# Kernel tuning notes

Hardware: AMD Instinct MI355X
Metric: run time of the kernel (lower is better)

## Reference

```python
import jax, jax.numpy as jnp
import numpy as np
from jax.ops import segment_sum, segment_max

B, L, D, H, DK, NL, V, FF = 8, 256, 256, 8, 32, 4, 2048, 1024
N = B * L
EPS = 1e-5


def _ln(x, g, b):
    m = jnp.mean(x, -1, keepdims=True)
    v = jnp.var(x, -1, keepdims=True)
    return (x - m) * jax.lax.rsqrt(v + EPS) * g + b


def setup_inputs() -> dict:
    key = jax.random.key(0)
    ks = list(jax.random.split(key, 16))
    # causal decoder-decoder edges, sorted by destination (DGL 'dd' eids)
    dst_seq = np.repeat(np.arange(L), np.arange(L) + 1)
    src_seq = np.concatenate([np.arange(j + 1) for j in range(L)])
    src = jnp.asarray(np.concatenate([src_seq + b * L for b in range(B)]), jnp.int32)
    dst = jnp.asarray(np.concatenate([dst_seq + b * L for b in range(B)]), jnp.int32)
    tokens = jax.random.randint(ks[0], (N,), 0, V)
    positions = jnp.tile(jnp.arange(L), B)  # tgt[1]
    s = 0.02
    nrm = lambda k, sh: jax.random.normal(k, sh, jnp.float32) * s
    return {
        'tokens': tokens, 'positions': positions, 'src': src, 'dst': dst,
        'value_tab': nrm(ks[1], (V, D)),
        'coord_tab': nrm(ks[2], (3, D)),
        'pos_tab': nrm(ks[3], (L, D)),
        'ln1_g': jnp.ones((NL, D), jnp.float32), 'ln1_b': jnp.zeros((NL, D), jnp.float32),
        'Wq': nrm(ks[4], (NL, D, D)), 'Wk': nrm(ks[5], (NL, D, D)),
        'Wv': nrm(ks[6], (NL, D, D)), 'Wo': nrm(ks[7], (NL, D, D)),
        'ln2_g': jnp.ones((NL, D), jnp.float32), 'ln2_b': jnp.zeros((NL, D), jnp.float32),
        'W1': nrm(ks[8], (NL, D, FF)), 'b1': jnp.zeros((NL, FF), jnp.float32),
        'W2': nrm(ks[9], (NL, FF, D)), 'b2': jnp.zeros((NL, D), jnp.float32),
        'lnf_g': jnp.ones((D,), jnp.float32), 'lnf_b': jnp.zeros((D,), jnp.float32),
        'Wgen': nrm(ks[10], (D, V)), 'bgen': jnp.zeros((V,), jnp.float32),
    }


def reference(tokens, positions, src, dst, value_tab, coord_tab, pos_tab,
              ln1_g, ln1_b, Wq, Wk, Wv, Wo, ln2_g, ln2_b,
              W1, b1, W2, b2, lnf_g, lnf_b, Wgen, bgen):
    # embeddings: value*sqrt(d) + coord(pos%3) + pos(pos//3)
    x = value_tab[tokens] * jnp.sqrt(jnp.float32(D)) \
        + coord_tab[positions % 3] + pos_tab[positions // 3]
    inv_sqrt_dk = 1.0 / jnp.sqrt(jnp.float32(DK))
    for i in range(NL):
        # pre_func: layernorm + qkv projection, split heads
        xn = _ln(x, ln1_g[i], ln1_b[i])
        q = (xn @ Wq[i]).reshape(N, H, DK)
        k = (xn @ Wk[i]).reshape(N, H, DK)
        v = (xn @ Wv[i]).reshape(N, H, DK)
        # apply_edges(u_dot_v): per-edge, per-head score
        score = jnp.einsum('ehd,ehd->eh', k[src], q[dst]) * inv_sqrt_dk  # [E,H]
        # edge_softmax over edges grouped by destination node
        m = jax.lax.stop_gradient(
            segment_max(score, dst, num_segments=N, indices_are_sorted=True))
        a = jnp.exp(score - m[dst])
        denom = segment_sum(a, dst, num_segments=N, indices_are_sorted=True)
        alpha = a / denom[dst]  # [E,H]
        # send_and_recv(u_mul_e -> sum): softmax-weighted aggregation
        z = segment_sum(v[src] * alpha[..., None], dst,
                        num_segments=N, indices_are_sorted=True).reshape(N, D)
        # post_func: output proj + residual, then FFN sublayer
        x = x + z @ Wo[i]
        xn2 = _ln(x, ln2_g[i], ln2_b[i])
        x = x + (jax.nn.relu(xn2 @ W1[i] + b1[i]) @ W2[i] + b2[i])
    x = _ln(x, lnf_g, lnf_b)
    return jax.nn.log_softmax(x @ Wgen + bgen, axis=-1)  # generator
```

## Files before the change

kernel.cpp:

```cpp
#include <hip/hip_runtime.h>
#include <hip/hip_bf16.h>
#include <math.h>

constexpr int B_ = 8, L_ = 256, D_ = 256, H_ = 8, DK_ = 32, NL_ = 4, V_ = 2048, FF_ = 1024;
constexpr int N_ = B_ * L_;
constexpr float EPS_ = 1e-5f;

typedef short bf16x8 __attribute__((ext_vector_type(8)));
typedef float f32x4 __attribute__((ext_vector_type(4)));
typedef _Float16 f16x4 __attribute__((ext_vector_type(4)));

__device__ __forceinline__ short f2b(float f) {
    union { __hip_bfloat16 h; short s; } u;
    u.h = __float2bfloat16(f);
    return u.s;
}

__device__ __forceinline__ void load16_lds(const void* g, void* l) {
    auto gp = reinterpret_cast<const __attribute__((address_space(1))) unsigned int*>(
        reinterpret_cast<unsigned long long>(g));
    auto lp = reinterpret_cast<__attribute__((address_space(3))) unsigned int*>(
        (unsigned int)reinterpret_cast<unsigned long long>(l));
    __builtin_amdgcn_global_load_lds(gp, lp, 16, 0, 0);
}

__global__ void embed_kernel(const int* __restrict__ tokens, const int* __restrict__ positions,
                             const float* __restrict__ vtab, const float* __restrict__ ctab,
                             const float* __restrict__ ptab, float* __restrict__ x) {
    int n = blockIdx.x, d = threadIdx.x;
    int tok = tokens[n], p = positions[n];
    x[n * D_ + d] = vtab[tok * D_ + d] * 16.0f + ctab[(p % 3) * D_ + d] + ptab[(p / 3) * D_ + d];
}

__global__ void ln_kernel(const float* __restrict__ x, const float* __restrict__ g,
                          const float* __restrict__ b, short* __restrict__ out) {
    __shared__ float r1[4], r2[4], mv[2];
    int n = blockIdx.x, t = threadIdx.x;
    float v = x[n * D_ + t];
    float s1 = v, s2 = v * v;
#pragma unroll
    for (int off = 32; off; off >>= 1) {
        s1 += __shfl_down(s1, off, 64);
        s2 += __shfl_down(s2, off, 64);
    }
    int w = t >> 6;
    if ((t & 63) == 0) { r1[w] = s1; r2[w] = s2; }
    __syncthreads();
    if (t == 0) {
        float a = r1[0] + r1[1] + r1[2] + r1[3];
        float c = r2[0] + r2[1] + r2[2] + r2[3];
        float mean = a * (1.0f / D_);
        float var = c * (1.0f / D_) - mean * mean;
        mv[0] = mean;
        mv[1] = rsqrtf(var + EPS_);
    }
    __syncthreads();
    out[n * D_ + t] = f2b((v - mv[0]) * mv[1] * g[t] + b[t]);
}

__global__ void transpose_w(const float* __restrict__ src, short* __restrict__ dst, int K, int Nn) {
    __shared__ float tile[32][33];
    int n0 = blockIdx.x * 32, k0 = blockIdx.y * 32;
    size_t base = (size_t)blockIdx.z * K * Nn;
    src += base;
    dst += base;
    int tx = threadIdx.x, ty = threadIdx.y;
#pragma unroll
    for (int i = 0; i < 32; i += 8)
        tile[ty + i][tx] = src[(size_t)(k0 + ty + i) * Nn + n0 + tx];
    __syncthreads();
#pragma unroll
    for (int i = 0; i < 32; i += 8)
        dst[(size_t)(n0 + ty + i) * K + k0 + tx] = f2b(tile[tx][ty + i]);
}

__global__ void transpose_w4(const float* __restrict__ Wq, const float* __restrict__ Wk,
                             const float* __restrict__ Wv, const float* __restrict__ Wo,
                             short* __restrict__ wqT, short* __restrict__ wkT,
                             short* __restrict__ wvT, short* __restrict__ woT) {
    __shared__ float tile[32][33];
    int z = blockIdx.z, m = z & 3, layer = z >> 2;
    const float* src = (m == 0) ? Wq : (m == 1) ? Wk : (m == 2) ? Wv : Wo;
    short* dst = (m == 0) ? wqT : (m == 1) ? wkT : (m == 2) ? wvT : woT;
    src += (size_t)layer * D_ * D_;
    dst += (size_t)layer * D_ * D_;
    int n0 = blockIdx.x * 32, k0 = blockIdx.y * 32;
    int tx = threadIdx.x, ty = threadIdx.y;
#pragma unroll
    for (int i = 0; i < 32; i += 8)
        tile[ty + i][tx] = src[(size_t)(k0 + ty + i) * D_ + n0 + tx];
    __syncthreads();
#pragma unroll
    for (int i = 0; i < 32; i += 8)
        dst[(size_t)(n0 + ty + i) * D_ + k0 + tx] = f2b(tile[tx][ty + i]);
}

template <int EPI, bool HAS_BIAS>
__device__ __forceinline__ void gemm_body(short (*As)[64], short (*Bs)[64],
                                          const short* __restrict__ A, const short* __restrict__ Bt,
                                          const float* __restrict__ bias, float* __restrict__ Cf,
                                          short* __restrict__ Cb, int M, int K, int Nout,
                                          int kbeg, int kend, int kz) {
    int t = threadIdx.x;
    int m0 = blockIdx.x * 64, n0 = blockIdx.y * 64;
    int lane = t & 63, w = t >> 6;
    int mo = (w & 1) * 32, no = (w >> 1) * 32;
    int quad = lane >> 4, r = lane & 15;
    f32x4 acc00 = {}, acc01 = {}, acc10 = {}, acc11 = {};
    int srow = 16 * w + (lane >> 3);
    int scol = (lane & 7) * 8;
    const short* Ag = &A[(size_t)(m0 + srow) * K + scol];
    const short* Bg = &Bt[(size_t)(n0 + srow) * K + scol];
    for (int k0 = kbeg; k0 < kend; k0 += 64) {
        __syncthreads();
        load16_lds(Ag + k0, &As[16 * w][0]);
        load16_lds(Ag + (size_t)8 * K + k0, &As[16 * w + 8][0]);
        load16_lds(Bg + k0, &Bs[16 * w][0]);
        load16_lds(Bg + (size_t)8 * K + k0, &Bs[16 * w + 8][0]);
        __syncthreads();
#pragma unroll
        for (int kk = 0; kk < 64; kk += 32) {
            bf16x8 a0 = *(const bf16x8*)&As[mo + r][kk + quad * 8];
            bf16x8 a1 = *(const bf16x8*)&As[mo + 16 + r][kk + quad * 8];
            bf16x8 b0 = *(const bf16x8*)&Bs[no + r][kk + quad * 8];
            bf16x8 b1 = *(const bf16x8*)&Bs[no + 16 + r][kk + quad * 8];
            acc00 = __builtin_amdgcn_mfma_f32_16x16x32_bf16(a0, b0, acc00, 0, 0, 0);
            acc01 = __builtin_amdgcn_mfma_f32_16x16x32_bf16(a0, b1, acc01, 0, 0, 0);
            acc10 = __builtin_amdgcn_mfma_f32_16x16x32_bf16(a1, b0, acc10, 0, 0, 0);
            acc11 = __builtin_amdgcn_mfma_f32_16x16x32_bf16(a1, b1, acc11, 0, 0, 0);
        }
    }
#pragma unroll
    for (int i = 0; i < 2; ++i) {
#pragma unroll
        for (int j = 0; j < 2; ++j) {
            f32x4 acc = (i == 0) ? (j == 0 ? acc00 : acc01) : (j == 0 ? acc10 : acc11);
            int col = n0 + no + j * 16 + r;
            float bval = HAS_BIAS ? bias[col] : 0.f;
#pragma unroll
            for (int p = 0; p < 4; ++p) {
                int row = m0 + mo + i * 16 + quad * 4 + p;
                float v = acc[p];
                if (EPI == 0) {
                    Cf[(size_t)row * Nout + col] = v;
                } else if (EPI == 1) {
                    Cb[(size_t)row * Nout + col] = f2b(fmaxf(v + bval, 0.f));
                } else if (EPI == 2) {
                    float add = v + ((HAS_BIAS && kz == 0) ? bval : 0.f);
                    atomicAdd(&Cf[(size_t)row * Nout + col], add);
                } else if (EPI == 3) {
                    Cf[(size_t)row * Nout + col] = v + bval;
                } else if (EPI == 4) {
                    Cb[(size_t)row * Nout + col] = f2b(v);
                } else {
                    ((_Float16*)Cb)[(size_t)row * Nout + col] = (_Float16)v;
                }
            }
        }
    }
}

__global__ __launch_bounds__(256) void gemm_qkv(const short* __restrict__ A, const short* __restrict__ wq,
                                                const short* __restrict__ wk, const short* __restrict__ wv,
                                                short* __restrict__ q, short* __restrict__ k,
                                                short* __restrict__ v, int M, int K, int Nout) {
    __shared__ short As[64][64];
    __shared__ short Bs[64][64];
    if (blockIdx.z == 0)
        gemm_body<4, false>(As, Bs, A, wq, nullptr, nullptr, q, M, K, Nout, 0, K, 0);
    else if (blockIdx.z == 1)
        gemm_body<4, false>(As, Bs, A, wk, nullptr, nullptr, k, M, K, Nout, 0, K, 0);
    else
        gemm_body<5, false>(As, Bs, A, wv, nullptr, nullptr, v, M, K, Nout, 0, K, 0);
}

template <int SPLITK, bool HAS_BIAS>
__global__ __launch_bounds__(256) void gemm_accum(const short* __restrict__ A, const short* __restrict__ Bt,
                                                  const float* __restrict__ bias, float* __restrict__ C,
                                                  int M, int K, int Nout) {
    __shared__ short As[64][64];
    __shared__ short Bs[64][64];
    int Kp = K / SPLITK;
    int kz = blockIdx.z;
    gemm_body<2, HAS_BIAS>(As, Bs, A, Bt, bias, C, nullptr, M, K, Nout, kz * Kp, kz * Kp + Kp, kz);
}

__global__ __launch_bounds__(256) void gemm_biasrelu_bf16(const short* __restrict__ A,
                                                          const short* __restrict__ Bt,
                                                          const float* __restrict__ bias,
                                                          short* __restrict__ C, int M, int K, int Nout) {
    __shared__ short As[64][64];
    __shared__ short Bs[64][64];
    gemm_body<1, true>(As, Bs, A, Bt, bias, nullptr, C, M, K, Nout, 0, K, 0);
}

__global__ __launch_bounds__(256) void gemm_bias(const short* __restrict__ A, const short* __restrict__ Bt,
                                                 const float* __restrict__ bias, float* __restrict__ C,
                                                 int M, int K, int Nout) {
    __shared__ short As[64][64];
    __shared__ short Bs[64][64];
    gemm_body<3, true>(As, Bs, A, Bt, bias, C, nullptr, M, K, Nout, 0, K, 0);
}

__global__ __launch_bounds__(64) void attn_kernel(const short* __restrict__ q,
                                                  const short* __restrict__ k,
                                                  const _Float16* __restrict__ v,
                                                  short* __restrict__ z) {
    int blk = blockIdx.x;
    int bh = blk & 63;
    int qt = 15 - (blk >> 6);
    int b = bh >> 3, h = bh & 7;
    int lane = threadIdx.x;
    int r = lane & 15, quad = lane >> 4;
    int row0 = b * L_;

    bf16x8 qf = *(const bf16x8*)&q[(size_t)(row0 + qt * 16 + r) * D_ + h * DK_ + quad * 8];
    f32x4 O0 = {}, O1 = {};
    float mA = -1e30f, den = 0.f;
    int nk = qt + 1;

    bf16x8 kf = *(const bf16x8*)&k[(size_t)(row0 + r) * D_ + h * DK_ + quad * 8];
    f16x4 va, vb;
    {
        const _Float16* vp = v + (size_t)(row0 + quad * 4) * D_ + h * DK_;
#pragma unroll
        for (int i = 0; i < 4; ++i) {
            va[i] = vp[(size_t)i * D_ + r];
            vb[i] = vp[(size_t)i * D_ + 16 + r];
        }
    }
    for (int kt = 0; kt < nk; ++kt) {
        bf16x8 kf_n = kf;
        f16x4 va_n = va, vb_n = vb;
        if (kt + 1 < nk) {
            kf_n = *(const bf16x8*)&k[(size_t)(row0 + (kt + 1) * 16 + r) * D_ + h * DK_ + quad * 8];
            const _Float16* vp = v + (size_t)(row0 + (kt + 1) * 16 + quad * 4) * D_ + h * DK_;
#pragma unroll
            for (int i = 0; i < 4; ++i) {
                va_n[i] = vp[(size_t)i * D_ + r];
                vb_n[i] = vp[(size_t)i * D_ + 16 + r];
            }
        }
        f32x4 zero = {};
        f32x4 s = __builtin_amdgcn_mfma_f32_16x16x32_bf16(kf, qf, zero, 0, 0, 0);
#pragma unroll
        for (int i2 = 0; i2 < 4; ++i2) s[i2] *= 0.17677669529663687f;
        if (kt == qt) {
#pragma unroll
            for (int i2 = 0; i2 < 4; ++i2)
                if (quad * 4 + i2 > r) s[i2] = -1e30f;
        }
        float tmax = fmaxf(fmaxf(s[0], s[1]), fmaxf(s[2], s[3]));
        tmax = fmaxf(tmax, __shfl_xor(tmax, 16, 64));
        tmax = fmaxf(tmax, __shfl_xor(tmax, 32, 64));
        float mn = fmaxf(mA, tmax);
        float alpha = __expf(mA - mn);
        mA = mn;
        float p0 = __expf(s[0] - mn), p1 = __expf(s[1] - mn);
        float p2 = __expf(s[2] - mn), p3 = __expf(s[3] - mn);
        float ts = (p0 + p1) + (p2 + p3);
        ts += __shfl_xor(ts, 16, 64);
        ts += __shfl_xor(ts, 32, 64);
        den = den * alpha + ts;
        f16x4 pf;
        pf[0] = (_Float16)p0; pf[1] = (_Float16)p1; pf[2] = (_Float16)p2; pf[3] = (_Float16)p3;
        float al[4];
#pragma unroll
        for (int i2 = 0; i2 < 4; ++i2) al[i2] = __shfl(alpha, quad * 4 + i2, 64);
#pragma unroll
        for (int i2 = 0; i2 < 4; ++i2) { O0[i2] *= al[i2]; O1[i2] *= al[i2]; }
        O0 = __builtin_amdgcn_mfma_f32_16x16x16f16(pf, va, O0, 0, 0, 0);
        O1 = __builtin_amdgcn_mfma_f32_16x16x16f16(pf, vb, O1, 0, 0, 0);
        kf = kf_n; va = va_n; vb = vb_n;
    }
#pragma unroll
    for (int i2 = 0; i2 < 4; ++i2) {
        float inv = 1.0f / __shfl(den, quad * 4 + i2, 64);
        int rowz = row0 + qt * 16 + quad * 4 + i2;
        z[(size_t)rowz * D_ + h * DK_ + r] = f2b(O0[i2] * inv);
        z[(size_t)rowz * D_ + h * DK_ + 16 + r] = f2b(O1[i2] * inv);
    }
}

__global__ void lsm_kernel(float* __restrict__ logits) {
    __shared__ float rm[4], rs[4];
    int row = blockIdx.x, t = threadIdx.x;
    float* p = logits + (size_t)row * V_;
    float vals[8];
    float mx = -INFINITY;
#pragma unroll
    for (int i = 0; i < 8; ++i) {
        vals[i] = p[t + i * 256];
        mx = fmaxf(mx, vals[i]);
    }
#pragma unroll
    for (int off = 32; off; off >>= 1) mx = fmaxf(mx, __shfl_xor(mx, off, 64));
    int w = t >> 6;
    if ((t & 63) == 0) rm[w] = mx;
    __syncthreads();
    mx = fmaxf(fmaxf(rm[0], rm[1]), fmaxf(rm[2], rm[3]));
    float s = 0.f;
#pragma unroll
    for (int i = 0; i < 8; ++i) s += __expf(vals[i] - mx);
#pragma unroll
    for (int off = 32; off; off >>= 1) s += __shfl_xor(s, off, 64);
    if ((t & 63) == 0) rs[w] = s;
    __syncthreads();
    s = rs[0] + rs[1] + rs[2] + rs[3];
    float lse = mx + logf(s);
#pragma unroll
    for (int i = 0; i < 8; ++i) p[t + i * 256] = vals[i] - lse;
}

extern "C" void kernel_launch(void* const* d_in, const int* in_sizes, int n_in,
                              void* d_out, int out_size, void* d_ws, size_t ws_size,
                              hipStream_t stream) {
    const int* tokens = (const int*)d_in[0];
    const int* positions = (const int*)d_in[1];
    const float* vtab = (const float*)d_in[4];
    const float* ctab = (const float*)d_in[5];
    const float* ptab = (const float*)d_in[6];
    const float* ln1_g = (const float*)d_in[7];
    const float* ln1_b = (const float*)d_in[8];
    const float* Wq = (const float*)d_in[9];
    const float* Wk = (const float*)d_in[10];
    const float* Wv = (const float*)d_in[11];
    const float* Wo = (const float*)d_in[12];
    const float* ln2_g = (const float*)d_in[13];
    const float* ln2_b = (const float*)d_in[14];
    const float* W1 = (const float*)d_in[15];
    const float* b1 = (const float*)d_in[16];
    const float* W2 = (const float*)d_in[17];
    const float* b2 = (const float*)d_in[18];
    const float* lnf_g = (const float*)d_in[19];
    const float* lnf_b = (const float*)d_in[20];
    const float* Wgen = (const float*)d_in[21];
    const float* bgen = (const float*)d_in[22];

    char* p = (char*)d_ws;
    float* x = (float*)p;      p += (size_t)N_ * D_ * 4;
    short* qb = (short*)p;     p += (size_t)N_ * D_ * 4;
    short* kb = (short*)p;     p += (size_t)N_ * D_ * 4;
    short* vbh = (short*)p;    p += (size_t)N_ * D_ * 4;
    short* xnb = (short*)p;    p += (size_t)N_ * D_ * 2;
    short* zbb = (short*)p;    p += (size_t)N_ * D_ * 2;
    short* hbb = (short*)p;    p += (size_t)N_ * FF_ * 2;
    short* wqT = (short*)p;    p += (size_t)NL_ * D_ * D_ * 2;
    short* wkT = (short*)p;    p += (size_t)NL_ * D_ * D_ * 2;
    short* wvT = (short*)p;    p += (size_t)NL_ * D_ * D_ * 2;
    short* woT = (short*)p;    p += (size_t)NL_ * D_ * D_ * 2;
    short* w1T = (short*)p;    p += (size_t)NL_ * D_ * FF_ * 2;
    short* w2T = (short*)p;    p += (size_t)NL_ * FF_ * D_ * 2;
    short* wgT = (short*)p;    p += (size_t)D_ * V_ * 2;
    float* out = (float*)d_out;

    dim3 tb(32, 8);
    transpose_w4<<<dim3(8, 8, 16), tb, 0, stream>>>(Wq, Wk, Wv, Wo, wqT, wkT, wvT, woT);
    transpose_w<<<dim3(32, 8, NL_), tb, 0, stream>>>(W1, w1T, D_, FF_);
    transpose_w<<<dim3(8, 32, NL_), tb, 0, stream>>>(W2, w2T, FF_, D_);
    transpose_w<<<dim3(64, 8, 1), tb, 0, stream>>>(Wgen, wgT, D_, V_);

    embed_kernel<<<N_, 256, 0, stream>>>(tokens, positions, vtab, ctab, ptab, x);
    dim3 gQKV(N_ / 64, D_ / 64, 3);
    dim3 gWo(N_ / 64, D_ / 64, 4);
    dim3 gW1(N_ / 64, FF_ / 64);
    dim3 gW2(N_ / 64, D_ / 64, 8);
    dim3 gGen(N_ / 64, V_ / 64);
    for (int i = 0; i < NL_; ++i) {
        ln_kernel<<<N_, 256, 0, stream>>>(x, ln1_g + i * D_, ln1_b + i * D_, xnb);
        gemm_qkv<<<gQKV, 256, 0, stream>>>(xnb, wqT + (size_t)i * D_ * D_, wkT + (size_t)i * D_ * D_,
                                           wvT + (size_t)i * D_ * D_, qb, kb, vbh, N_, D_, D_);
        attn_kernel<<<B_ * H_ * 16, 64, 0, stream>>>(qb, kb, (const _Float16*)vbh, zbb);
        gemm_accum<4, false><<<gWo, 256, 0, stream>>>(zbb, woT + (size_t)i * D_ * D_, nullptr, x, N_, D_, D_);
        ln_kernel<<<N_, 256, 0, stream>>>(x, ln2_g + i * D_, ln2_b + i * D_, xnb);
        gemm_biasrelu_bf16<<<gW1, 256, 0, stream>>>(xnb, w1T + (size_t)i * D_ * FF_, b1 + (size_t)i * FF_,
                                                    hbb, N_, D_, FF_);
        gemm_accum<8, true><<<gW2, 256, 0, stream>>>(hbb, w2T + (size_t)i * FF_ * D_, b2 + (size_t)i * D_,
                                                     x, N_, FF_, D_);
    }
    ln_kernel<<<N_, 256, 0, stream>>>(x, lnf_g, lnf_b, xnb);
    gemm_bias<<<gGen, 256, 0, stream>>>(xnb, wgT, bgen, out, N_, D_, V_);
    lsm_kernel<<<N_, 256, 0, stream>>>(out);
}
```

Measured before the change: 361.1 us.

## Add 128x128 GEMM for W1/generator, register-prefetch small GEMMs, halve split-K

```diff
diff --git a/kernel.cpp b/kernel.cpp
--- a/kernel.cpp
+++ b/kernel.cpp
@@ -96,10 +96,10 @@
 }
 
 template <int EPI, bool HAS_BIAS>
-__device__ __forceinline__ void gemm_body(short (*As)[64], short (*Bs)[64],
+__device__ __forceinline__ void gemm_body(short (*As)[40], short (*Bs)[40],
                                           const short* __restrict__ A, const short* __restrict__ Bt,
                                           const float* __restrict__ bias, float* __restrict__ Cf,
-                                          short* __restrict__ Cb, int M, int K, int Nout,
+                                          short* __restrict__ Cb, int K, int Nout,
                                           int kbeg, int kend, int kz) {
     int t = threadIdx.x;
     int m0 = blockIdx.x * 64, n0 = blockIdx.y * 64;
@@ -107,28 +107,28 @@
     int mo = (w & 1) * 32, no = (w >> 1) * 32;
     int quad = lane >> 4, r = lane & 15;
     f32x4 acc00 = {}, acc01 = {}, acc10 = {}, acc11 = {};
-    int srow = 16 * w + (lane >> 3);
-    int scol = (lane & 7) * 8;
-    const short* Ag = &A[(size_t)(m0 + srow) * K + scol];
-    const short* Bg = &Bt[(size_t)(n0 + srow) * K + scol];
-    for (int k0 = kbeg; k0 < kend; k0 += 64) {
+    int sr = t >> 2, sc = (t & 3) * 8;
+    const short* Ap = &A[(size_t)(m0 + sr) * K + sc];
+    const short* Bg = &Bt[(size_t)(n0 + sr) * K + sc];
+    int4 aR = *(const int4*)(Ap + kbeg);
+    int4 bR = *(const int4*)(Bg + kbeg);
+    for (int k0 = kbeg; k0 < kend; k0 += 32) {
         __syncthreads();
-        load16_lds(Ag + k0, &As[16 * w][0]);
-        load16_lds(Ag + (size_t)8 * K + k0, &As[16 * w + 8][0]);
-        load16_lds(Bg + k0, &Bs[16 * w][0]);
-        load16_lds(Bg + (size_t)8 * K + k0, &Bs[16 * w + 8][0]);
+        *(int4*)&As[sr][sc] = aR;
+        *(int4*)&Bs[sr][sc] = bR;
         __syncthreads();
-#pragma unroll
-        for (int kk = 0; kk < 64; kk += 32) {
-            bf16x8 a0 = *(const bf16x8*)&As[mo + r][kk + quad * 8];
-            bf16x8 a1 = *(const bf16x8*)&As[mo + 16 + r][kk + quad * 8];
-            bf16x8 b0 = *(const bf16x8*)&Bs[no + r][kk + quad * 8];
-            bf16x8 b1 = *(const bf16x8*)&Bs[no + 16 + r][kk + quad * 8];
-            acc00 = __builtin_amdgcn_mfma_f32_16x16x32_bf16(a0, b0, acc00, 0, 0, 0);
-            acc01 = __builtin_amdgcn_mfma_f32_16x16x32_bf16(a0, b1, acc01, 0, 0, 0);
-            acc10 = __builtin_amdgcn_mfma_f32_16x16x32_bf16(a1, b0, acc10, 0, 0, 0);
-            acc11 = __builtin_amdgcn_mfma_f32_16x16x32_bf16(a1, b1, acc11, 0, 0, 0);
-        }
+        if (k0 + 32 < kend) {
+            aR = *(const int4*)(Ap + k0 + 32);
+            bR = *(const int4*)(Bg + k0 + 32);
+        }
+        bf16x8 a0 = *(const bf16x8*)&As[mo + r][quad * 8];
+        bf16x8 a1 = *(const bf16x8*)&As[mo + 16 + r][quad * 8];
+        bf16x8 b0 = *(const bf16x8*)&Bs[no + r][quad * 8];
+        bf16x8 b1 = *(const bf16x8*)&Bs[no + 16 + r][quad * 8];
+        acc00 = __builtin_amdgcn_mfma_f32_16x16x32_bf16(a0, b0, acc00, 0, 0, 0);
+        acc01 = __builtin_amdgcn_mfma_f32_16x16x32_bf16(a0, b1, acc01, 0, 0, 0);
+        acc10 = __builtin_amdgcn_mfma_f32_16x16x32_bf16(a1, b0, acc10, 0, 0, 0);
+        acc11 = __builtin_amdgcn_mfma_f32_16x16x32_bf16(a1, b1, acc11, 0, 0, 0);
     }
 #pragma unroll
     for (int i = 0; i < 2; ++i) {
@@ -141,15 +141,9 @@
             for (int p = 0; p < 4; ++p) {
                 int row = m0 + mo + i * 16 + quad * 4 + p;
                 float v = acc[p];
-                if (EPI == 0) {
-                    Cf[(size_t)row * Nout + col] = v;
-                } else if (EPI == 1) {
-                    Cb[(size_t)row * Nout + col] = f2b(fmaxf(v + bval, 0.f));
-                } else if (EPI == 2) {
+                if (EPI == 2) {
                     float add = v + ((HAS_BIAS && kz == 0) ? bval : 0.f);
                     atomicAdd(&Cf[(size_t)row * Nout + col], add);
-                } else if (EPI == 3) {
-                    Cf[(size_t)row * Nout + col] = v + bval;
                 } else if (EPI == 4) {
                     Cb[(size_t)row * Nout + col] = f2b(v);
                 } else {
@@ -163,43 +157,83 @@
 __global__ __launch_bounds__(256) void gemm_qkv(const short* __restrict__ A, const short* __restrict__ wq,
                                                 const short* __restrict__ wk, const short* __restrict__ wv,
                                                 short* __restrict__ q, short* __restrict__ k,
-                                                short* __restrict__ v, int M, int K, int Nout) {
-    __shared__ short As[64][64];
-    __shared__ short Bs[64][64];
+                                                short* __restrict__ v, int K, int Nout) {
+    __shared__ short As[64][40];
+    __shared__ short Bs[64][40];
     if (blockIdx.z == 0)
-        gemm_body<4, false>(As, Bs, A, wq, nullptr, nullptr, q, M, K, Nout, 0, K, 0);
+        gemm_body<4, false>(As, Bs, A, wq, nullptr, nullptr, q, K, Nout, 0, K, 0);
     else if (blockIdx.z == 1)
-        gemm_body<4, false>(As, Bs, A, wk, nullptr, nullptr, k, M, K, Nout, 0, K, 0);
+        gemm_body<4, false>(As, Bs, A, wk, nullptr, nullptr, k, K, Nout, 0, K, 0);
     else
-        gemm_body<5, false>(As, Bs, A, wv, nullptr, nullptr, v, M, K, Nout, 0, K, 0);
+        gemm_body<5, false>(As, Bs, A, wv, nullptr, nullptr, v, K, Nout, 0, K, 0);
 }
 
 template <int SPLITK, bool HAS_BIAS>
 __global__ __launch_bounds__(256) void gemm_accum(const short* __restrict__ A, const short* __restrict__ Bt,
                                                   const float* __restrict__ bias, float* __restrict__ C,
-                                                  int M, int K, int Nout) {
-    __shared__ short As[64][64];
-    __shared__ short Bs[64][64];
+                                                  int K, int Nout) {
+    __shared__ short As[64][40];
+    __shared__ short Bs[64][40];
     int Kp = K / SPLITK;
     int kz = blockIdx.z;
-    gemm_body<2, HAS_BIAS>(As, Bs, A, Bt, bias, C, nullptr, M, K, Nout, kz * Kp, kz * Kp + Kp, kz);
-}
-
-__global__ __launch_bounds__(256) void gemm_biasrelu_bf16(const short* __restrict__ A,
-                                                          const short* __restrict__ Bt,
-                                                          const float* __restrict__ bias,
-                                                          short* __restrict__ C, int M, int K, int Nout) {
-    __shared__ short As[64][64];
-    __shared__ short Bs[64][64];
-    gemm_body<1, true>(As, Bs, A, Bt, bias, nullptr, C, M, K, Nout, 0, K, 0);
-}
-
-__global__ __launch_bounds__(256) void gemm_bias(const short* __restrict__ A, const short* __restrict__ Bt,
-                                                 const float* __restrict__ bias, float* __restrict__ C,
-                                                 int M, int K, int Nout) {
-    __shared__ short As[64][64];
-    __shared__ short Bs[64][64];
-    gemm_body<3, true>(As, Bs, A, Bt, bias, C, nullptr, M, K, Nout, 0, K, 0);
+    gemm_body<2, HAS_BIAS>(As, Bs, A, Bt, bias, C, nullptr, K, Nout, kz * Kp, kz * Kp + Kp, kz);
+}
+
+template <int EPI>
+__global__ __launch_bounds__(256) void gemm128(const short* __restrict__ A, const short* __restrict__ Bt,
+                                               const float* __restrict__ bias, float* __restrict__ Cf,
+                                               short* __restrict__ Cb, int K, int Nout) {
+    __shared__ short As[128][64];
+    __shared__ short Bs[128][64];
+    int t = threadIdx.x;
+    int m0 = blockIdx.x * 128, n0 = blockIdx.y * 128;
+    int lane = t & 63, w = t >> 6;
+    int wr = (w & 1) * 64, wc = (w >> 1) * 64;
+    int quad = lane >> 4, r = lane & 15;
+    f32x4 acc[4][4] = {};
+    int srow = lane >> 3, scol = (lane & 7) * 8;
+    const short* Ag = &A[(size_t)(m0 + 32 * w + srow) * K + scol];
+    const short* Bg = &Bt[(size_t)(n0 + 32 * w + srow) * K + scol];
+    for (int k0 = 0; k0 < K; k0 += 64) {
+        __syncthreads();
+#pragma unroll
+        for (int op = 0; op < 4; ++op) {
+            load16_lds(Ag + (size_t)(8 * op) * K + k0, &As[32 * w + 8 * op][0]);
+            load16_lds(Bg + (size_t)(8 * op) * K + k0, &Bs[32 * w + 8 * op][0]);
+        }
+        __syncthreads();
+#pragma unroll
+        for (int kk = 0; kk < 64; kk += 32) {
+            bf16x8 af[4], bf[4];
+#pragma unroll
+            for (int i = 0; i < 4; ++i) af[i] = *(const bf16x8*)&As[wr + i * 16 + r][kk + quad * 8];
+#pragma unroll
+            for (int j = 0; j < 4; ++j) bf[j] = *(const bf16x8*)&Bs[wc + j * 16 + r][kk + quad * 8];
+#pragma unroll
+            for (int i = 0; i < 4; ++i)
+#pragma unroll
+                for (int j = 0; j < 4; ++j)
+                    acc[i][j] = __builtin_amdgcn_mfma_f32_16x16x32_bf16(af[i], bf[j], acc[i][j], 0, 0, 0);
+        }
+    }
+#pragma unroll
+    for (int i = 0; i < 4; ++i) {
+#pragma unroll
+        for (int j = 0; j < 4; ++j) {
+            int col = n0 + wc + j * 16 + r;
+            float bval = bias[col];
+#pragma unroll
+            for (int p = 0; p < 4; ++p) {
+                int row = m0 + wr + i * 16 + quad * 4 + p;
+                float v = acc[i][j][p] + bval;
+                if (EPI == 1) {
+                    Cb[(size_t)row * Nout + col] = f2b(fmaxf(v, 0.f));
+                } else {
+                    Cf[(size_t)row * Nout + col] = v;
+                }
+            }
+        }
+    }
 }
 
 __global__ __launch_bounds__(64) void attn_kernel(const short* __restrict__ q,
@@ -339,9 +373,9 @@
 
     char* p = (char*)d_ws;
     float* x = (float*)p;      p += (size_t)N_ * D_ * 4;
-    short* qb = (short*)p;     p += (size_t)N_ * D_ * 4;
-    short* kb = (short*)p;     p += (size_t)N_ * D_ * 4;
-    short* vbh = (short*)p;    p += (size_t)N_ * D_ * 4;
+    short* qb = (short*)p;     p += (size_t)N_ * D_ * 2;
+    short* kb = (short*)p;     p += (size_t)N_ * D_ * 2;
+    short* vbh = (short*)p;    p += (size_t)N_ * D_ * 2;
     short* xnb = (short*)p;    p += (size_t)N_ * D_ * 2;
     short* zbb = (short*)p;    p += (size_t)N_ * D_ * 2;
     short* hbb = (short*)p;    p += (size_t)N_ * FF_ * 2;
@@ -362,23 +396,23 @@
 
     embed_kernel<<<N_, 256, 0, stream>>>(tokens, positions, vtab, ctab, ptab, x);
     dim3 gQKV(N_ / 64, D_ / 64, 3);
-    dim3 gWo(N_ / 64, D_ / 64, 4);
-    dim3 gW1(N_ / 64, FF_ / 64);
-    dim3 gW2(N_ / 64, D_ / 64, 8);
-    dim3 gGen(N_ / 64, V_ / 64);
+    dim3 gWo(N_ / 64, D_ / 64, 2);
+    dim3 gW1(N_ / 128, FF_ / 128);
+    dim3 gW2(N_ / 64, D_ / 64, 4);
+    dim3 gGen(N_ / 128, V_ / 128);
     for (int i = 0; i < NL_; ++i) {
         ln_kernel<<<N_, 256, 0, stream>>>(x, ln1_g + i * D_, ln1_b + i * D_, xnb);
         gemm_qkv<<<gQKV, 256, 0, stream>>>(xnb, wqT + (size_t)i * D_ * D_, wkT + (size_t)i * D_ * D_,
-                                           wvT + (size_t)i * D_ * D_, qb, kb, vbh, N_, D_, D_);
+                                           wvT + (size_t)i * D_ * D_, qb, kb, vbh, D_, D_);
         attn_kernel<<<B_ * H_ * 16, 64, 0, stream>>>(qb, kb, (const _Float16*)vbh, zbb);
-        gemm_accum<4, false><<<gWo, 256, 0, stream>>>(zbb, woT + (size_t)i * D_ * D_, nullptr, x, N_, D_, D_);
+        gemm_accum<2, false><<<gWo, 256, 0, stream>>>(zbb, woT + (size_t)i * D_ * D_, nullptr, x, D_, D_);
         ln_kernel<<<N_, 256, 0, stream>>>(x, ln2_g + i * D_, ln2_b + i * D_, xnb);
-        gemm_biasrelu_bf16<<<gW1, 256, 0, stream>>>(xnb, w1T + (size_t)i * D_ * FF_, b1 + (size_t)i * FF_,
-                                                    hbb, N_, D_, FF_);
-        gemm_accum<8, true><<<gW2, 256, 0, stream>>>(hbb, w2T + (size_t)i * FF_ * D_, b2 + (size_t)i * D_,
-                                                     x, N_, FF_, D_);
+        gemm128<1><<<gW1, 256, 0, stream>>>(xnb, w1T + (size_t)i * D_ * FF_, b1 + (size_t)i * FF_,
+                                            nullptr, hbb, D_, FF_);
+        gemm_accum<4, true><<<gW2, 256, 0, stream>>>(hbb, w2T + (size_t)i * FF_ * D_, b2 + (size_t)i * D_,
+                                                     x, FF_, D_);
     }
     ln_kernel<<<N_, 256, 0, stream>>>(x, lnf_g, lnf_b, xnb);
-    gemm_bias<<<gGen, 256, 0, stream>>>(xnb, wgT, bgen, out, N_, D_, V_);
+    gemm128<3><<<gGen, 256, 0, stream>>>(xnb, wgT, bgen, out, nullptr, D_, V_);
     lsm_kernel<<<N_, 256, 0, stream>>>(out);
 }
```

Result: faster. 338.3 us (-6.3%).
